# Optimization experiments

Hardware: AMD Instinct MI355X
Metric: run time of the kernel (lower is better)

The kernel has to match this reference:

```python
import jax, jax.numpy as jnp
import numpy as np

EPS = 0.1

def setup_inputs() -> dict:
    key = jax.random.key(0)
    k1, k2, k3, k4, k5, k6 = jax.random.split(key, 6)
    B, N, Cin, Cout = 8, 2048, 128, 128
    x = jax.random.normal(k1, (B, N, Cin), dtype=jnp.float32)
    x_0 = jax.random.normal(k2, (B, N, Cout), dtype=jnp.float32)
    adj = jax.random.randint(k3, (B, N, N), 0, 2, dtype=jnp.int32)
    # learned parameters (Linear without bias stores weight [out,in]; we keep [in,out])
    W_lin = jax.random.normal(k4, (Cin, Cout), dtype=jnp.float32) / np.sqrt(Cin)
    w_att_l = jax.random.normal(k5, (Cout,), dtype=jnp.float32) / np.sqrt(Cout)
    w_att_r = jax.random.normal(k6, (Cout,), dtype=jnp.float32) / np.sqrt(Cout)
    return {"x": x, "x_0": x_0, "adj": adj, "W_lin": W_lin, "w_att_l": w_att_l, "w_att_r": w_att_r}

def reference(x, x_0, adj, W_lin, w_att_l, w_att_r):
    # x: [B,N,Cin] -> h: [B,N,Cout]
    h = jnp.einsum('bni,io->bno', x, W_lin)
    alpha_l = jnp.einsum('bno,o->bn', h, w_att_l)  # [B,N]
    alpha_r = jnp.einsum('bno,o->bn', h, w_att_r)  # [B,N]
    # alpha[b,i,j] = tanh(alpha_r[b,i] * alpha_l[b,j])
    alpha = jnp.tanh(alpha_r[:, :, None] * alpha_l[:, None, :])  # [B,N,N]
    alpha = jnp.where(adj == 0, jnp.float32(0.0), alpha)
    # dropout p=0.0 -> identity
    out = jnp.einsum('bij,bjo->bio', alpha, h)  # [B,N,Cout]
    return out + EPS * x_0
```

## Files before the change

kernel.cpp:

```cpp
#include <hip/hip_runtime.h>
#include <stdint.h>

#define B_   8
#define N_   2048
#define C_   128
#define EPS_ 0.1f

typedef __attribute__((ext_vector_type(8))) short short8;
typedef __attribute__((ext_vector_type(4))) float f32x4;

__device__ __forceinline__ unsigned short f2bf(float f) {
    union { float f; uint32_t u; } v; v.f = f;
    uint32_t u = v.u + 0x7FFF + ((v.u >> 16) & 1);
    return (unsigned short)(u >> 16);
}

__global__ __launch_bounds__(128) void k_wt(const float* __restrict__ W,
                                            unsigned short* __restrict__ Wt) {
    const int o = blockIdx.x, k = threadIdx.x;
    Wt[o * C_ + k] = f2bf(W[k * C_ + o]);
}

__global__ __launch_bounds__(256) void k_h(
    const float* __restrict__ x, const unsigned short* __restrict__ Wt,
    const float* __restrict__ wl, const float* __restrict__ wr,
    unsigned short* __restrict__ ht, float* __restrict__ al, float* __restrict__ ar)
{
    const int b    = blockIdx.x >> 5;
    const int i0   = (blockIdx.x & 31) * 64;
    const int t    = threadIdx.x;
    const int lane = t & 63;
    const int wid  = t >> 6;

    __shared__ __align__(16) unsigned short xs[64 * 128];
    __shared__ __align__(16) unsigned short ws[128 * 128];

    #pragma unroll
    for (int p = 0; p < 4; ++p) {
        const int s = p * 256 + t, row = s >> 4, u = s & 15;
        const float* gp = x + ((size_t)(b * N_ + i0 + row) * C_ + u * 8);
        float4 f0 = *(const float4*)gp;
        float4 f1 = *(const float4*)(gp + 4);
        short8 tv;
        tv[0] = (short)f2bf(f0.x); tv[1] = (short)f2bf(f0.y);
        tv[2] = (short)f2bf(f0.z); tv[3] = (short)f2bf(f0.w);
        tv[4] = (short)f2bf(f1.x); tv[5] = (short)f2bf(f1.y);
        tv[6] = (short)f2bf(f1.z); tv[7] = (short)f2bf(f1.w);
        *(short8*)&xs[row * 128 + (u ^ (row & 15)) * 8] = tv;
    }
    #pragma unroll
    for (int p = 0; p < 8; ++p) {
        const int s = p * 256 + t, o = s >> 4, u = s & 15;
        int4 v = *(const int4*)(Wt + o * C_ + u * 8);
        *(int4*)&ws[o * 128 + (u ^ (o & 15)) * 8] = v;
    }
    __syncthreads();

    const int m0 = wid * 16, lr = lane & 15, q = lane >> 4;
    f32x4 acc[8];
    #pragma unroll
    for (int i = 0; i < 8; ++i) acc[i] = (f32x4){0.f, 0.f, 0.f, 0.f};

    #pragma unroll
    for (int s = 0; s < 4; ++s) {
        const int m = m0 + lr;
        short8 af = *(const short8*)&xs[m * 128 + ((s * 4 + q) ^ (m & 15)) * 8];
        #pragma unroll
        for (int tt = 0; tt < 8; ++tt) {
            const int o = tt * 16 + lr;
            short8 bf = *(const short8*)&ws[o * 128 + ((s * 4 + q) ^ (o & 15)) * 8];
            acc[tt] = __builtin_amdgcn_mfma_f32_16x16x32_bf16(af, bf, acc[tt], 0, 0, 0);
        }
    }

    float pl[4] = {0.f, 0.f, 0.f, 0.f}, pr[4] = {0.f, 0.f, 0.f, 0.f};
    const int j0 = i0 + m0 + q * 4;
    #pragma unroll
    for (int tt = 0; tt < 8; ++tt) {
        const int o = tt * 16 + lr;
        const float wlv = wl[o], wrv = wr[o];
        unsigned int lo = (unsigned int)f2bf(acc[tt][0]) | ((unsigned int)f2bf(acc[tt][1]) << 16);
        unsigned int hi = (unsigned int)f2bf(acc[tt][2]) | ((unsigned int)f2bf(acc[tt][3]) << 16);
        uint2 u2; u2.x = lo; u2.y = hi;
        *(uint2*)&ht[((size_t)(b * C_ + o)) * N_ + j0] = u2;
        #pragma unroll
        for (int r = 0; r < 4; ++r) {
            pl[r] = fmaf(acc[tt][r], wlv, pl[r]);
            pr[r] = fmaf(acc[tt][r], wrv, pr[r]);
        }
    }
    #pragma unroll
    for (int msk = 1; msk < 16; msk <<= 1) {
        #pragma unroll
        for (int r = 0; r < 4; ++r) {
            pl[r] += __shfl_xor(pl[r], msk, 64);
            pr[r] += __shfl_xor(pr[r], msk, 64);
        }
    }
    if (lr == 0) {
        #pragma unroll
        for (int r = 0; r < 4; ++r) {
            al[b * N_ + j0 + r] = pl[r];
            ar[b * N_ + j0 + r] = pr[r];
        }
    }
}

struct Pref {
    int4   a0, a1;
    int4   h0, h1;
    float4 l0, l1;
};

__global__ __launch_bounds__(512) void k_out(
    const int* __restrict__ adj, const unsigned short* __restrict__ ht,
    const float* __restrict__ al, const float* __restrict__ ar,
    const float* __restrict__ x0, float* __restrict__ out)
{
    const int b    = blockIdx.x >> 5;
    const int i0   = (blockIdx.x & 31) * 64;
    const int t    = threadIdx.x;
    const int lane = t & 63;
    const int wid  = t >> 6;

    __shared__ __align__(16) unsigned short a_s[64 * 64];
    __shared__ __align__(16) unsigned short h_s[128 * 64];

    const int arow = t >> 3;
    const int jq   = t & 7;
    const float arv = ar[b * N_ + i0 + arow];
    const int ho1 = t >> 3;

    auto ldc = [&](int c) -> Pref {
        Pref P;
        const int j0 = c * 64;
        const int* ap = adj + ((size_t)(b * N_) + i0 + arow) * N_ + j0 + jq * 8;
        P.a0 = *(const int4*)ap;
        P.a1 = *(const int4*)(ap + 4);
        const unsigned short* hp = ht + (size_t)b * C_ * N_ + j0 + jq * 8;
        P.h0 = *(const int4*)(hp + (size_t)ho1 * N_);
        P.h1 = *(const int4*)(hp + (size_t)(ho1 + 64) * N_);
        const float* alp = al + b * N_ + j0 + jq * 8;
        P.l0 = *(const float4*)alp;
        P.l1 = *(const float4*)(alp + 4);
        return P;
    };

    auto stage = [&](const Pref& P) {
        short8 pk;
        const int*   av = (const int*)&P.a0;
        const int*   bv = (const int*)&P.a1;
        const float* af = (const float*)&P.l0;
        const float* bf = (const float*)&P.l1;
        #pragma unroll
        for (int e = 0; e < 4; ++e) {
            float z  = arv * af[e];
            float ex = __expf(2.f * z);
            float th = 1.f - 2.f / (ex + 1.f);
            pk[e] = av[e] ? (short)f2bf(th) : (short)0;
        }
        #pragma unroll
        for (int e = 0; e < 4; ++e) {
            float z  = arv * bf[e];
            float ex = __expf(2.f * z);
            float th = 1.f - 2.f / (ex + 1.f);
            pk[4 + e] = bv[e] ? (short)f2bf(th) : (short)0;
        }
        *(short8*)&a_s[arow * 64 + (jq ^ (arow & 7)) * 8] = pk;
        *(int4*)&h_s[ho1 * 64 + (jq ^ (ho1 & 7)) * 8]        = P.h0;
        *(int4*)&h_s[(ho1 + 64) * 64 + (jq ^ (ho1 & 7)) * 8] = P.h1;
    };

    const int m0 = (wid & 3) * 16, n0 = (wid >> 2) * 64;
    const int lr = lane & 15, q = lane >> 4;
    f32x4 acc[4];
    #pragma unroll
    for (int i = 0; i < 4; ++i) acc[i] = (f32x4){0.f, 0.f, 0.f, 0.f};

    auto mma = [&]() {
        #pragma unroll
        for (int s2 = 0; s2 < 2; ++s2) {
            const int m = m0 + lr;
            short8 afr = *(const short8*)&a_s[m * 64 + ((s2 * 4 + q) ^ (m & 7)) * 8];
            #pragma unroll
            for (int tt = 0; tt < 4; ++tt) {
                const int o = n0 + tt * 16 + lr;
                short8 bfr = *(const short8*)&h_s[o * 64 + ((s2 * 4 + q) ^ (o & 7)) * 8];
                acc[tt] = __builtin_amdgcn_mfma_f32_16x16x32_bf16(afr, bfr, acc[tt], 0, 0, 0);
            }
        }
    };

    Pref p0 = ldc(0);
    Pref p1 = ldc(1);

    for (int cc = 0; cc < 16; ++cc) {
        __syncthreads();
        stage(p0);
        if (cc < 15) p0 = ldc(2 * cc + 2);
        __syncthreads();
        mma();

        __syncthreads();
        stage(p1);
        if (cc < 15) p1 = ldc(2 * cc + 3);
        __syncthreads();
        mma();
    }

    #pragma unroll
    for (int tt = 0; tt < 4; ++tt) {
        const int o = n0 + tt * 16 + lr;
        #pragma unroll
        for (int r = 0; r < 4; ++r) {
            const int row = i0 + m0 + q * 4 + r;
            const size_t idx = ((size_t)(b * N_) + row) * C_ + o;
            out[idx] = acc[tt][r] + EPS_ * x0[idx];
        }
    }
}

extern "C" void kernel_launch(void* const* d_in, const int* in_sizes, int n_in,
                              void* d_out, int out_size, void* d_ws, size_t ws_size,
                              hipStream_t stream) {
    const float* x   = (const float*)d_in[0];
    const float* x0  = (const float*)d_in[1];
    const int*   adj = (const int*)d_in[2];
    const float* W   = (const float*)d_in[3];
    const float* wl  = (const float*)d_in[4];
    const float* wr  = (const float*)d_in[5];
    float* out = (float*)d_out;

    unsigned short* ht = (unsigned short*)d_ws;
    float* al = (float*)((char*)d_ws + (size_t)B_ * C_ * N_ * 2);
    float* ar = al + B_ * N_;
    unsigned short* Wt = (unsigned short*)(ar + B_ * N_);

    k_wt <<<C_,             C_,  0, stream>>>(W, Wt);
    k_h  <<<B_ * (N_ / 64), 256, 0, stream>>>(x, Wt, wl, wr, ht, al, ar);
    k_out<<<B_ * (N_ / 64), 512, 0, stream>>>(adj, ht, al, ar, x0, out);
}
```

Measured before the change: 235.1 us.

## Double-buffer LDS in aggregation kernel and halve row tile to 32

The output kernel now uses two LDS buffers so staging the next adjacency/h chunk overlaps the MFMA on the current one, cutting from four barriers per chunk pair to two. The row tile per block shrinks from 64 to 32 with 256 threads, doubling the grid to 512 blocks for better CU occupancy. In exchange, each block reloads the full h tile for fewer rows, which doubles total h traffic from L2, and each thread holds more prefetch registers.

Result: faster. 228.4 us (-2.8%).

```diff
diff --git a/kernel.cpp b/kernel.cpp
--- a/kernel.cpp
+++ b/kernel.cpp
@@ -108,28 +108,27 @@
 
 struct Pref {
     int4   a0, a1;
-    int4   h0, h1;
+    int4   h0, h1, h2, h3;
     float4 l0, l1;
 };
 
-__global__ __launch_bounds__(512) void k_out(
+__global__ __launch_bounds__(256) void k_out(
     const int* __restrict__ adj, const unsigned short* __restrict__ ht,
     const float* __restrict__ al, const float* __restrict__ ar,
     const float* __restrict__ x0, float* __restrict__ out)
 {
-    const int b    = blockIdx.x >> 5;
-    const int i0   = (blockIdx.x & 31) * 64;
+    const int b    = blockIdx.x >> 6;
+    const int i0   = (blockIdx.x & 63) * 32;
     const int t    = threadIdx.x;
     const int lane = t & 63;
     const int wid  = t >> 6;
 
-    __shared__ __align__(16) unsigned short a_s[64 * 64];
-    __shared__ __align__(16) unsigned short h_s[128 * 64];
+    __shared__ __align__(16) unsigned short a_s[2][32 * 64];
+    __shared__ __align__(16) unsigned short h_s[2][128 * 64];
 
     const int arow = t >> 3;
     const int jq   = t & 7;
     const float arv = ar[b * N_ + i0 + arow];
-    const int ho1 = t >> 3;
 
     auto ldc = [&](int c) -> Pref {
         Pref P;
@@ -138,15 +137,17 @@
         P.a0 = *(const int4*)ap;
         P.a1 = *(const int4*)(ap + 4);
         const unsigned short* hp = ht + (size_t)b * C_ * N_ + j0 + jq * 8;
-        P.h0 = *(const int4*)(hp + (size_t)ho1 * N_);
-        P.h1 = *(const int4*)(hp + (size_t)(ho1 + 64) * N_);
+        P.h0 = *(const int4*)(hp + (size_t)arow * N_);
+        P.h1 = *(const int4*)(hp + (size_t)(arow + 32) * N_);
+        P.h2 = *(const int4*)(hp + (size_t)(arow + 64) * N_);
+        P.h3 = *(const int4*)(hp + (size_t)(arow + 96) * N_);
         const float* alp = al + b * N_ + j0 + jq * 8;
         P.l0 = *(const float4*)alp;
         P.l1 = *(const float4*)(alp + 4);
         return P;
     };
 
-    auto stage = [&](const Pref& P) {
+    auto stage = [&](int buf, const Pref& P) {
         short8 pk;
         const int*   av = (const int*)&P.a0;
         const int*   bv = (const int*)&P.a1;
@@ -166,46 +167,54 @@
             float th = 1.f - 2.f / (ex + 1.f);
             pk[4 + e] = bv[e] ? (short)f2bf(th) : (short)0;
         }
-        *(short8*)&a_s[arow * 64 + (jq ^ (arow & 7)) * 8] = pk;
-        *(int4*)&h_s[ho1 * 64 + (jq ^ (ho1 & 7)) * 8]        = P.h0;
-        *(int4*)&h_s[(ho1 + 64) * 64 + (jq ^ (ho1 & 7)) * 8] = P.h1;
+        const int su = (jq ^ (arow & 7)) * 8;
+        *(short8*)&a_s[buf][arow * 64 + su] = pk;
+        *(int4*)&h_s[buf][(arow)      * 64 + su] = P.h0;
+        *(int4*)&h_s[buf][(arow + 32) * 64 + su] = P.h1;
+        *(int4*)&h_s[buf][(arow + 64) * 64 + su] = P.h2;
+        *(int4*)&h_s[buf][(arow + 96) * 64 + su] = P.h3;
     };
 
-    const int m0 = (wid & 3) * 16, n0 = (wid >> 2) * 64;
+    const int m0 = (wid & 1) * 16, n0 = (wid >> 1) * 64;
     const int lr = lane & 15, q = lane >> 4;
     f32x4 acc[4];
     #pragma unroll
     for (int i = 0; i < 4; ++i) acc[i] = (f32x4){0.f, 0.f, 0.f, 0.f};
 
-    auto mma = [&]() {
+    auto mma = [&](int buf) {
         #pragma unroll
         for (int s2 = 0; s2 < 2; ++s2) {
             const int m = m0 + lr;
-            short8 afr = *(const short8*)&a_s[m * 64 + ((s2 * 4 + q) ^ (m & 7)) * 8];
+            short8 afr = *(const short8*)&a_s[buf][m * 64 + ((s2 * 4 + q) ^ (m & 7)) * 8];
             #pragma unroll
             for (int tt = 0; tt < 4; ++tt) {
                 const int o = n0 + tt * 16 + lr;
-                short8 bfr = *(const short8*)&h_s[o * 64 + ((s2 * 4 + q) ^ (o & 7)) * 8];
+                short8 bfr = *(const short8*)&h_s[buf][o * 64 + ((s2 * 4 + q) ^ (o & 7)) * 8];
                 acc[tt] = __builtin_amdgcn_mfma_f32_16x16x32_bf16(afr, bfr, acc[tt], 0, 0, 0);
             }
         }
     };
 
-    Pref p0 = ldc(0);
-    Pref p1 = ldc(1);
+    {
+        Pref p = ldc(0);
+        stage(0, p);
+    }
+    Pref pA = ldc(1);
+    Pref pB = ldc(2);
+    __syncthreads();
 
     for (int cc = 0; cc < 16; ++cc) {
+        stage(1, pA);
+        if (cc < 15) pA = ldc(2 * cc + 3);
+        mma(0);
         __syncthreads();
-        stage(p0);
-        if (cc < 15) p0 = ldc(2 * cc + 2);
+
+        if (cc < 15) {
+            stage(0, pB);
+            if (cc < 14) pB = ldc(2 * cc + 4);
+        }
+        mma(1);
         __syncthreads();
-        mma();
-
-        __syncthreads();
-        stage(p1);
-        if (cc < 15) p1 = ldc(2 * cc + 3);
-        __syncthreads();
-        mma();
     }
 
     #pragma unroll
@@ -238,5 +247,5 @@
 
     k_wt <<<C_,             C_,  0, stream>>>(W, Wt);
     k_h  <<<B_ * (N_ / 64), 256, 0, stream>>>(x, Wt, wl, wr, ht, al, ar);
-    k_out<<<B_ * (N_ / 64), 512, 0, stream>>>(adj, ht, al, ar, x0, out);
-}
+    k_out<<<B_ * (N_ / 32), 256, 0, stream>>>(adj, ht, al, ar, x0, out);
+}
```

## Load MFMA operands directly from global memory, dropping LDS staging and barriers

Applied to the files above, without the earlier changes.

The output kernel no longer stages the masked attention tile and h tile through shared memory with block barriers. Each wave now loads its adjacency, alpha_l and h fragments straight into registers in MFMA operand layout, double-buffered across 32-column steps. Tiles shrink to 32 rows per block with 256 threads and two blocks per CU, and the tanh division becomes a hardware reciprocal. The cost is redundant global loads: each h fragment is now fetched by both row-waves, and alpha_l by every wave, with nothing shared through LDS.

Measured after the change: 283.1 us. 1.2x slower.

```diff
diff --git a/kernel.cpp b/kernel.cpp
--- a/kernel.cpp
+++ b/kernel.cpp
@@ -106,116 +106,87 @@
     }
 }
 
-struct Pref {
+struct PrefO {
     int4   a0, a1;
-    int4   h0, h1;
     float4 l0, l1;
+    int4   h0, h1, h2, h3;
 };
 
-__global__ __launch_bounds__(512) void k_out(
+__global__ __launch_bounds__(256, 2) void k_out(
     const int* __restrict__ adj, const unsigned short* __restrict__ ht,
     const float* __restrict__ al, const float* __restrict__ ar,
     const float* __restrict__ x0, float* __restrict__ out)
 {
-    const int b    = blockIdx.x >> 5;
-    const int i0   = (blockIdx.x & 31) * 64;
+    const int b    = blockIdx.x >> 6;
+    const int i0   = (blockIdx.x & 63) * 32;
     const int t    = threadIdx.x;
     const int lane = t & 63;
     const int wid  = t >> 6;
-
-    __shared__ __align__(16) unsigned short a_s[64 * 64];
-    __shared__ __align__(16) unsigned short h_s[128 * 64];
-
-    const int arow = t >> 3;
-    const int jq   = t & 7;
-    const float arv = ar[b * N_ + i0 + arow];
-    const int ho1 = t >> 3;
-
-    auto ldc = [&](int c) -> Pref {
-        Pref P;
-        const int j0 = c * 64;
-        const int* ap = adj + ((size_t)(b * N_) + i0 + arow) * N_ + j0 + jq * 8;
-        P.a0 = *(const int4*)ap;
-        P.a1 = *(const int4*)(ap + 4);
-        const unsigned short* hp = ht + (size_t)b * C_ * N_ + j0 + jq * 8;
-        P.h0 = *(const int4*)(hp + (size_t)ho1 * N_);
-        P.h1 = *(const int4*)(hp + (size_t)(ho1 + 64) * N_);
-        const float* alp = al + b * N_ + j0 + jq * 8;
-        P.l0 = *(const float4*)alp;
-        P.l1 = *(const float4*)(alp + 4);
+    const int m0   = (wid & 1) * 16, n0 = (wid >> 1) * 64;
+    const int r    = lane & 15, q = lane >> 4;
+
+    const int row  = i0 + m0 + r;
+    const float arv = ar[b * N_ + row];
+
+    const int*            adjp = adj + ((size_t)(b * N_ + row)) * N_ + q * 8;
+    const float*          alp  = al + b * N_ + q * 8;
+    const unsigned short* hb   = ht + (size_t)b * C_ * N_ + q * 8;
+    const unsigned short* hp0  = hb + (size_t)(n0 +  0 + r) * N_;
+    const unsigned short* hp1  = hb + (size_t)(n0 + 16 + r) * N_;
+    const unsigned short* hp2  = hb + (size_t)(n0 + 32 + r) * N_;
+    const unsigned short* hp3  = hb + (size_t)(n0 + 48 + r) * N_;
+
+    auto ld = [&](int s) -> PrefO {
+        PrefO P; const int jb = s * 32;
+        P.a0 = *(const int4*)(adjp + jb);
+        P.a1 = *(const int4*)(adjp + jb + 4);
+        P.l0 = *(const float4*)(alp + jb);
+        P.l1 = *(const float4*)(alp + jb + 4);
+        P.h0 = *(const int4*)(hp0 + jb);
+        P.h1 = *(const int4*)(hp1 + jb);
+        P.h2 = *(const int4*)(hp2 + jb);
+        P.h3 = *(const int4*)(hp3 + jb);
         return P;
     };
 
-    auto stage = [&](const Pref& P) {
-        short8 pk;
+    f32x4 acc[4];
+    #pragma unroll
+    for (int i = 0; i < 4; ++i) acc[i] = (f32x4){0.f, 0.f, 0.f, 0.f};
+
+    auto step = [&](const PrefO& P) {
         const int*   av = (const int*)&P.a0;
-        const int*   bv = (const int*)&P.a1;
-        const float* af = (const float*)&P.l0;
-        const float* bf = (const float*)&P.l1;
-        #pragma unroll
-        for (int e = 0; e < 4; ++e) {
-            float z  = arv * af[e];
+        const float* lv = (const float*)&P.l0;
+        short8 af;
+        #pragma unroll
+        for (int e = 0; e < 8; ++e) {
+            float z  = arv * lv[e];
             float ex = __expf(2.f * z);
-            float th = 1.f - 2.f / (ex + 1.f);
-            pk[e] = av[e] ? (short)f2bf(th) : (short)0;
-        }
-        #pragma unroll
-        for (int e = 0; e < 4; ++e) {
-            float z  = arv * bf[e];
-            float ex = __expf(2.f * z);
-            float th = 1.f - 2.f / (ex + 1.f);
-            pk[4 + e] = bv[e] ? (short)f2bf(th) : (short)0;
-        }
-        *(short8*)&a_s[arow * 64 + (jq ^ (arow & 7)) * 8] = pk;
-        *(int4*)&h_s[ho1 * 64 + (jq ^ (ho1 & 7)) * 8]        = P.h0;
-        *(int4*)&h_s[(ho1 + 64) * 64 + (jq ^ (ho1 & 7)) * 8] = P.h1;
+            float th = 1.f - 2.f * __builtin_amdgcn_rcpf(ex + 1.f);
+            af[e] = av[e] ? (short)f2bf(th) : (short)0;
+        }
+        acc[0] = __builtin_amdgcn_mfma_f32_16x16x32_bf16(af, *(const short8*)&P.h0, acc[0], 0, 0, 0);
+        acc[1] = __builtin_amdgcn_mfma_f32_16x16x32_bf16(af, *(const short8*)&P.h1, acc[1], 0, 0, 0);
+        acc[2] = __builtin_amdgcn_mfma_f32_16x16x32_bf16(af, *(const short8*)&P.h2, acc[2], 0, 0, 0);
+        acc[3] = __builtin_amdgcn_mfma_f32_16x16x32_bf16(af, *(const short8*)&P.h3, acc[3], 0, 0, 0);
     };
 
-    const int m0 = (wid & 3) * 16, n0 = (wid >> 2) * 64;
-    const int lr = lane & 15, q = lane >> 4;
-    f32x4 acc[4];
-    #pragma unroll
-    for (int i = 0; i < 4; ++i) acc[i] = (f32x4){0.f, 0.f, 0.f, 0.f};
-
-    auto mma = [&]() {
-        #pragma unroll
-        for (int s2 = 0; s2 < 2; ++s2) {
-            const int m = m0 + lr;
-            short8 afr = *(const short8*)&a_s[m * 64 + ((s2 * 4 + q) ^ (m & 7)) * 8];
-            #pragma unroll
-            for (int tt = 0; tt < 4; ++tt) {
-                const int o = n0 + tt * 16 + lr;
-                short8 bfr = *(const short8*)&h_s[o * 64 + ((s2 * 4 + q) ^ (o & 7)) * 8];
-                acc[tt] = __builtin_amdgcn_mfma_f32_16x16x32_bf16(afr, bfr, acc[tt], 0, 0, 0);
-            }
-        }
-    };
-
-    Pref p0 = ldc(0);
-    Pref p1 = ldc(1);
-
-    for (int cc = 0; cc < 16; ++cc) {
-        __syncthreads();
-        stage(p0);
-        if (cc < 15) p0 = ldc(2 * cc + 2);
-        __syncthreads();
-        mma();
-
-        __syncthreads();
-        stage(p1);
-        if (cc < 15) p1 = ldc(2 * cc + 3);
-        __syncthreads();
-        mma();
+    PrefO A = ld(0);
+    PrefO Bp = ld(1);
+    for (int it = 0; it < 32; ++it) {
+        step(A);
+        if (it < 31) A = ld(2 * it + 2);
+        step(Bp);
+        if (it < 31) Bp = ld(2 * it + 3);
     }
 
     #pragma unroll
     for (int tt = 0; tt < 4; ++tt) {
-        const int o = n0 + tt * 16 + lr;
-        #pragma unroll
-        for (int r = 0; r < 4; ++r) {
-            const int row = i0 + m0 + q * 4 + r;
-            const size_t idx = ((size_t)(b * N_) + row) * C_ + o;
-            out[idx] = acc[tt][r] + EPS_ * x0[idx];
+        const int o = n0 + tt * 16 + r;
+        #pragma unroll
+        for (int rr = 0; rr < 4; ++rr) {
+            const int orow = i0 + m0 + q * 4 + rr;
+            const size_t idx = ((size_t)(b * N_) + orow) * C_ + o;
+            out[idx] = acc[tt][rr] + EPS_ * x0[idx];
         }
     }
 }
@@ -238,5 +209,5 @@
 
     k_wt <<<C_,             C_,  0, stream>>>(W, Wt);
     k_h  <<<B_ * (N_ / 64), 256, 0, stream>>>(x, Wt, wl, wr, ht, al, ar);
-    k_out<<<B_ * (N_ / 64), 512, 0, stream>>>(adj, ht, al, ar, x0, out);
-}
+    k_out<<<B_ * (N_ / 32), 256, 0, stream>>>(adj, ht, al, ar, x0, out);
+}
```
